# Performance work log

Measured on AMD Instinct MI355X. Metric: run time of the kernel, lower is better.

Reference implementation:

```python
import jax, jax.numpy as jnp
import numpy as np

D_MODEL, H, D_FF = 512, 8, 2048
B, S = 2, 2048
EPS = 1e-6


def _layernorm(x, alpha, beta):
    # Faithful to the torch module: unbiased std (ddof=1), eps added to STD,
    # scalar alpha/beta parameters.
    m = jnp.mean(x, axis=-1, keepdims=True)
    var = jnp.sum((x - m) ** 2, axis=-1, keepdims=True) / (x.shape[-1] - 1)
    std = jnp.sqrt(var)
    return alpha * (x - m) / (std + EPS) + beta


def _mha(x, mask, Wq, bq, Wk, bk, Wv, bv, Wo, bo):
    Bn, Sn, D = x.shape
    dk = D // H
    q = (x @ Wq + bq).reshape(Bn, Sn, H, dk).transpose(0, 2, 1, 3)  # [B,H,S,dk]
    k = (x @ Wk + bk).reshape(Bn, Sn, H, dk).transpose(0, 2, 1, 3)
    v = (x @ Wv + bv).reshape(Bn, Sn, H, dk).transpose(0, 2, 1, 3)
    scores = jnp.einsum('bhqd,bhkd->bhqk', q, k) / jnp.sqrt(jnp.float32(dk))
    scores = jnp.where(mask == 0, -jnp.inf, scores)  # mask [B,1,1,S] broadcasts
    attn = jax.nn.softmax(scores, axis=-1)
    out = jnp.einsum('bhqk,bhkd->bhqd', attn, v)
    out = out.transpose(0, 2, 1, 3).reshape(Bn, Sn, D)
    return out @ Wo + bo


def _ffn(x, W1, b1, W2, b2):
    return jax.nn.relu(x @ W1 + b1) @ W2 + b2


def setup_inputs() -> dict:
    key = jax.random.key(0)
    ks = jax.random.split(key, 12)
    sd = 1.0 / np.sqrt(D_MODEL)
    sdf = 1.0 / np.sqrt(D_FF)
    inp = {
        'x': jax.random.normal(ks[0], (B, S, D_MODEL), jnp.float32),
        'src_mask': jnp.ones((B, 1, 1, S), jnp.int32),
        'Wq': jax.random.normal(ks[1], (D_MODEL, D_MODEL), jnp.float32) * sd,
        'bq': jnp.zeros((D_MODEL,), jnp.float32),
        'Wk': jax.random.normal(ks[2], (D_MODEL, D_MODEL), jnp.float32) * sd,
        'bk': jnp.zeros((D_MODEL,), jnp.float32),
        'Wv': jax.random.normal(ks[3], (D_MODEL, D_MODEL), jnp.float32) * sd,
        'bv': jnp.zeros((D_MODEL,), jnp.float32),
        'Wo': jax.random.normal(ks[4], (D_MODEL, D_MODEL), jnp.float32) * sd,
        'bo': jnp.zeros((D_MODEL,), jnp.float32),
        'W1': jax.random.normal(ks[5], (D_MODEL, D_FF), jnp.float32) * sd,
        'b1': jnp.zeros((D_FF,), jnp.float32),
        'W2': jax.random.normal(ks[6], (D_FF, D_MODEL), jnp.float32) * sdf,
        'b2': jnp.zeros((D_MODEL,), jnp.float32),
        'alpha1': jnp.ones((1,), jnp.float32),
        'beta1': jnp.zeros((1,), jnp.float32),
        'alpha2': jnp.ones((1,), jnp.float32),
        'beta2': jnp.zeros((1,), jnp.float32),
    }
    return inp


def reference(x, src_mask, Wq, bq, Wk, bk, Wv, bv, Wo, bo,
              W1, b1, W2, b2, alpha1, beta1, alpha2, beta2):
    # SkipConnection 0: x + dropout(MHA(LN(x)))  (dropout=0 -> identity)
    h1 = _layernorm(x, alpha1, beta1)
    x = x + _mha(h1, src_mask, Wq, bq, Wk, bk, Wv, bv, Wo, bo)
    # SkipConnection 1: x + dropout(FFN(LN(x)))
    h2 = _layernorm(x, alpha2, beta2)
    x = x + _ffn(h2, W1, b1, W2, b2)
    return x
```

## Files before the change

kernel.cpp:

```cpp
#include <hip/hip_runtime.h>
#include <hip/hip_bf16.h>

typedef __hip_bfloat16 bf16;
typedef __attribute__((ext_vector_type(8))) short s8v;
typedef __attribute__((ext_vector_type(4))) float f32x4;

#define DM 512
#define NH 8
#define DKH 64
#define DFF 2048
#define NB 2
#define NS 2048
#define NR (NB*NS)
#define LN_EPS 1e-6f
#define NEG_BIG (-1e30f)
#define LDQKV (3*DM)
#define SM_SHIFT (-6.0f)
#define PART_ELEMS (NB*NH*NS*DKH)

#define MFMA_B16(a,b,c) __builtin_amdgcn_mfma_f32_16x16x32_bf16(a,b,c,0,0,0)

#define GLOAD16(g, l) __builtin_amdgcn_global_load_lds( \
    (const __attribute__((address_space(1))) void*)(g), \
    (__attribute__((address_space(3))) void*)(l), 16, 0, 0)

__device__ __forceinline__ float us2f(unsigned int u){ return __uint_as_float(u << 16); }
__device__ __forceinline__ float b2f(bf16 v){ return __bfloat162float(v); }
__device__ __forceinline__ float ldf(const float* p){ return *p; }
__device__ __forceinline__ float ldf(const bf16* p){ return __bfloat162float(*p); }
__device__ __forceinline__ void stf(float* p, float v){ *p = v; }
__device__ __forceinline__ void stf(bf16* p, float v){ *p = __float2bfloat16(v); }
__device__ __forceinline__ unsigned short f2bu(float f){
  bf16 b = __float2bfloat16(f);
  return *reinterpret_cast<unsigned short*>(&b);
}

template<int N> __device__ __forceinline__ void waitcnt_vm(){
  if constexpr(N==0)      asm volatile("s_waitcnt vmcnt(0)" ::: "memory");
  else if constexpr(N==2) asm volatile("s_waitcnt vmcnt(2)" ::: "memory");
  else if constexpr(N==3) asm volatile("s_waitcnt vmcnt(3)" ::: "memory");
  else if constexpr(N==4) asm volatile("s_waitcnt vmcnt(4)" ::: "memory");
  else if constexpr(N==6) asm volatile("s_waitcnt vmcnt(6)" ::: "memory");
  else if constexpr(N==8) asm volatile("s_waitcnt vmcnt(8)" ::: "memory");
}

__device__ __forceinline__ int swz(int row, int colbyte){
  return ((row<<7) + colbyte) ^ ((row&7)<<4);
}

__device__ __forceinline__ float wsum(float v){
#pragma unroll
  for(int o=32;o>0;o>>=1) v += __shfl_down(v,o,64);
  return v;
}

template<int NTHR>
__device__ __forceinline__ void stage_tile(char* lds, const bf16* g, int ld, int R, int tid){
  int nch = R*8;
  for(int c = tid; c < nch; c += NTHR){
    int row = c>>3;
    int blk = (c&7) ^ (row&7);
    GLOAD16(g + (size_t)row*ld + blk*8, lds + c*16);
  }
}
__device__ __forceinline__ s8v read_frag(const char* lds, int row, int col){
  return *reinterpret_cast<const s8v*>(lds + swz(row, col<<1));
}

__global__ __launch_bounds__(256) void prep_kernel(
    const float* __restrict__ Wq, const float* __restrict__ Wk,
    const float* __restrict__ Wv, const float* __restrict__ Wo,
    const float* __restrict__ W1, const float* __restrict__ W2,
    bf16* __restrict__ WTqkv, bf16* __restrict__ WTo,
    bf16* __restrict__ WT1, bf16* __restrict__ WT2,
    const float* __restrict__ x, bf16* __restrict__ h1,
    const float* __restrict__ ap, const float* __restrict__ bp){
  __shared__ float t[64][65];
  __shared__ float s1[4], s2[4];
  int tid = threadIdx.x;
  if(blockIdx.x >= 768){
    int row = blockIdx.x - 768;
    const float* xr = x + (size_t)row*DM;
    float v0 = xr[tid], v1 = xr[tid+256];
    float s = wsum(v0+v1);
    float q = wsum(v0*v0+v1*v1);
    int wid = tid>>6, lane = tid&63;
    if(lane==0){ s1[wid]=s; s2[wid]=q; }
    __syncthreads();
    float S = s1[0]+s1[1]+s1[2]+s1[3];
    float Q = s2[0]+s2[1]+s2[2]+s2[3];
    float mean = S*(1.f/DM);
    float var  = (Q - (float)DM*mean*mean)*(1.f/(DM-1));
    float sd   = sqrtf(fmaxf(var,0.f));
    float sc = (*ap)/(sd+LN_EPS);
    float b = *bp;
    bf16* orow = h1 + (size_t)row*DM;
    orow[tid]     = __float2bfloat16((v0-mean)*sc + b);
    orow[tid+256] = __float2bfloat16((v1-mean)*sc + b);
    return;
  }
  int tb = blockIdx.x;
  const float* W; bf16* WT; int K, N, nx;
  if(tb < 192){
    int w = tb>>6; tb &= 63;
    W = (w==0)?Wq:(w==1)?Wk:Wv; WT = WTqkv + w*512*512; K=512; N=512; nx=8;
  } else if(tb < 256){ tb -= 192; W=Wo; WT=WTo; K=512; N=512; nx=8; }
  else if(tb < 512){ tb -= 256; W=W1; WT=WT1; K=512; N=2048; nx=32; }
  else { tb -= 512; W=W2; WT=WT2; K=2048; N=512; nx=8; }
  int n0 = (tb % nx)*64, k0 = (tb / nx)*64;
  int rr = tid>>6, cc = tid&63;
#pragma unroll
  for(int r=rr;r<64;r+=4) t[r][cc] = W[(size_t)(k0+r)*N + n0+cc];
  __syncthreads();
#pragma unroll
  for(int r=rr;r<64;r+=4) WT[(size_t)(n0+r)*K + k0+cc] = __float2bfloat16(t[cc][r]);
}

template<typename TI>
__global__ __launch_bounds__(256) void ln_kernel(const TI* __restrict__ x,
    bf16* __restrict__ out, const float* __restrict__ ap, const float* __restrict__ bp){
  __shared__ float s1[4], s2[4];
  int row = blockIdx.x, tid = threadIdx.x;
  const TI* xr = x + (size_t)row*DM;
  float v0 = ldf(xr+tid), v1 = ldf(xr+tid+256);
  float s = wsum(v0+v1);
  float q = wsum(v0*v0+v1*v1);
  int wid = tid>>6, lane = tid&63;
  if(lane==0){ s1[wid]=s; s2[wid]=q; }
  __syncthreads();
  float S = s1[0]+s1[1]+s1[2]+s1[3];
  float Q = s2[0]+s2[1]+s2[2]+s2[3];
  float mean = S*(1.f/DM);
  float var  = (Q - (float)DM*mean*mean)*(1.f/(DM-1));
  float sd   = sqrtf(fmaxf(var,0.f));
  float sc = (*ap)/(sd+LN_EPS);
  float b = *bp;
  bf16* orow = out + (size_t)row*DM;
  orow[tid]     = __float2bfloat16((v0-mean)*sc + b);
  orow[tid+256] = __float2bfloat16((v1-mean)*sc + b);
}

template<int BM, int BN, int RELU, int QKVSEL, typename TR, typename TO>
__global__ __launch_bounds__(256) void mfma_gemm(
    const bf16* __restrict__ A, const bf16* __restrict__ WT,
    const float* __restrict__ bias0, const float* __restrict__ bias1,
    const float* __restrict__ bias2,
    const TR* __restrict__ resid, TO* __restrict__ out,
    bf16* __restrict__ vt, int M, int N, int K){
  constexpr int NW = BN/2, NF = NW/16, MI = (BM+31)/32, WRS = BM/2;
  constexpr int LOADS = BM/32 + BN/32;
  __shared__ char lA[2][BM*128];
  __shared__ char lB[2][BN*128];
  int tid = threadIdx.x, wave = tid>>6, lane = tid&63;
  int m0 = blockIdx.x*BM, n0 = blockIdx.y*BN;
  int wr = wave>>1, wc = wave&1;
  int g = lane>>4, li = lane&15;
  f32x4 acc[MI][NF] = {};
  stage_tile<256>(lA[0], A + (size_t)m0*K, K, BM, tid);
  stage_tile<256>(lB[0], WT + (size_t)n0*K, K, BN, tid);
  int NT = K>>6;
  int cur = 0;
  for(int t=0; t<NT; ++t, cur^=1){
    if(t+1 < NT){
      stage_tile<256>(lA[cur^1], A + (size_t)m0*K + (t+1)*64, K, BM, tid);
      stage_tile<256>(lB[cur^1], WT + (size_t)n0*K + (t+1)*64, K, BN, tid);
      waitcnt_vm<LOADS>();
    } else {
      waitcnt_vm<0>();
    }
    __builtin_amdgcn_sched_barrier(0);
    __builtin_amdgcn_s_barrier();
    __builtin_amdgcn_sched_barrier(0);
#pragma unroll
    for(int kk=0; kk<2; kk++){
      s8v af[MI], bfr[NF];
#pragma unroll
      for(int mi=0;mi<MI;mi++) af[mi] = read_frag(lA[cur], wr*WRS+mi*16+li, kk*32+g*8);
#pragma unroll
      for(int ni=0;ni<NF;ni++) bfr[ni] = read_frag(lB[cur], wc*NW+ni*16+li, kk*32+g*8);
#pragma unroll
      for(int mi=0;mi<MI;mi++)
#pragma unroll
        for(int ni=0;ni<NF;ni++)
          acc[mi][ni] = MFMA_B16(af[mi], bfr[ni], acc[mi][ni]);
    }
    __builtin_amdgcn_sched_barrier(0);
    __builtin_amdgcn_s_barrier();
  }
#pragma unroll
  for(int mi=0;mi<MI;mi++)
#pragma unroll
  for(int ni=0;ni<NF;ni++){
    int row = m0 + wr*WRS + mi*16 + g*4;
    int col = n0 + wc*NW + ni*16 + li;
    const float* bp = bias0;
    if(QKVSEL) bp = (col<512)? bias0 : (col<1024)? (bias1-512) : (bias2-1024);
    float bb = bp[col];
    if(QKVSEL && col >= 1024){
      int hh = (col-1024)>>6, dd = (col-1024)&63;
      int b_ = row>>11, s = row&(NS-1);
      int kb_ = s&63;
      bf16* vtp = vt + (((size_t)(b_*NH+hh)*DKH + dd)*NS + (s&~63) + (kb_>>4));
#pragma unroll
      for(int r=0;r<4;r++)
        vtp[((kb_&15)+r)*4] = __float2bfloat16(acc[mi][ni][r] + bb);
      continue;
    }
#pragma unroll
    for(int r=0;r<4;r++){
      float v = acc[mi][ni][r] + bb;
      if(RELU) v = fmaxf(v, 0.f);
      size_t off = (size_t)(row+r)*N + col;
      if(resid) v += ldf(resid+off);
      stf(out+off, v);
    }
  }
}

__global__ __launch_bounds__(512,2) void flash_attn(
    const bf16* __restrict__ QKV, const bf16* __restrict__ VT,
    const int* __restrict__ mask, bf16* __restrict__ partA,
    bf16* __restrict__ partB, float* __restrict__ lbuf){
  __shared__ char lK[2][128*128];
  __shared__ char lV[2][2][64*128];
  __shared__ char lP[8][16*128];
  int tid = threadIdx.x, wave = tid>>6, lane = tid&63;
  int bid = blockIdx.x;
  int xcd = bid & 7, u = bid >> 3;
  int q0 = (u & 15)*128;
  int bhk = xcd + 8*(u>>4);
  int h = bhk & 7, kh = (bhk>>3)&1, b = bhk>>4;
  int kbase = kh*(NS/2);
  int g = lane>>4, li = lane&15;
  const bf16* Qg  = QKV + ((size_t)b*NS + q0)*LDQKV + h*DKH;
  const bf16* Kg  = QKV + ((size_t)b*NS + kbase)*LDQKV + DM + h*DKH;
  const bf16* VTg = VT + ((size_t)(b*NH + h))*DKH*NS + kbase;
  stage_tile<512>(lK[0], Qg, LDQKV, 128, tid);
  __syncthreads();
  s8v qf0 = read_frag(lK[0], wave*16+li, g*8);
  s8v qf1 = read_frag(lK[0], wave*16+li, 32+g*8);
  __syncthreads();
  stage_tile<512>(lK[0], Kg, LDQKV, 128, tid);
  stage_tile<512>(lV[0][0], VTg,      NS, 64, tid);
  stage_tile<512>(lV[0][1], VTg + 64, NS, 64, tid);
  unsigned long long mb = 0;
#pragma unroll 16
  for(int j=0;j<64;j++)
    mb |= (unsigned long long)(mask[b*NS + kbase + j*16 + li] != 0) << j;
  __syncthreads();
  f32x4 acc[4] = {};
  f32x4 acc_l = {};
  s8v ones;
#pragma unroll
  for(int j=0;j<8;j++) ones[j] = (short)0x3F80;
  char* lPw = lP[wave];

  auto compute = [&](int t, int c){
#pragma unroll
    for(int s=0;s<2;s++){
      f32x4 S[4] = {};
      __builtin_amdgcn_s_setprio(1);
#pragma unroll
      for(int kk=0;kk<2;kk++){
        s8v qf = kk ? qf1 : qf0;
        s8v kf[4];
#pragma unroll
        for(int ni=0;ni<4;ni++) kf[ni] = read_frag(lK[c], s*64+ni*16+li, kk*32+g*8);
#pragma unroll
        for(int ni=0;ni<4;ni++)
          S[ni] = MFMA_B16(qf, kf[ni], S[ni]);
      }
      __builtin_amdgcn_s_setprio(0);
      int jb = t*8 + s*4;
      float madd[4];
#pragma unroll
      for(int ni=0;ni<4;ni++)
        madd[ni] = ((mb>>(jb+ni))&1ull) ? SM_SHIFT : NEG_BIG;
#pragma unroll
      for(int r=0;r<4;r++){
        float e0 = __expf(fmaf(S[0][r], 0.125f, madd[0]));
        float e1 = __expf(fmaf(S[1][r], 0.125f, madd[1]));
        float e2 = __expf(fmaf(S[2][r], 0.125f, madd[2]));
        float e3 = __expf(fmaf(S[3][r], 0.125f, madd[3]));
        int row = g*4 + r;
        uint2 w;
        w.x = (unsigned int)f2bu(e0) | ((unsigned int)f2bu(e1)<<16);
        w.y = (unsigned int)f2bu(e2) | ((unsigned int)f2bu(e3)<<16);
        *reinterpret_cast<uint2*>(lPw + swz(row, li<<3)) = w;
      }
      __builtin_amdgcn_s_setprio(1);
#pragma unroll
      for(int kk=0;kk<2;kk++){
        s8v pf = read_frag(lPw, li, kk*32+g*8);
        s8v vf[4];
#pragma unroll
        for(int nd=0;nd<4;nd++) vf[nd] = read_frag(lV[c][s], nd*16+li, kk*32+g*8);
#pragma unroll
        for(int nd=0;nd<4;nd++)
          acc[nd] = MFMA_B16(pf, vf[nd], acc[nd]);
        acc_l = MFMA_B16(pf, ones, acc_l);
      }
      __builtin_amdgcn_s_setprio(0);
    }
  };

  int cur = 0;
  for(int t=0; t<7; ++t, cur^=1){
    stage_tile<512>(lK[cur^1], Kg + (size_t)(t+1)*128*LDQKV, LDQKV, 128, tid);
    stage_tile<512>(lV[cur^1][0], VTg + (t+1)*128,      NS, 64, tid);
    stage_tile<512>(lV[cur^1][1], VTg + (t+1)*128 + 64, NS, 64, tid);
    waitcnt_vm<4>();
    __builtin_amdgcn_sched_barrier(0);
    __builtin_amdgcn_s_barrier();
    __builtin_amdgcn_sched_barrier(0);
    compute(t, cur);
    __builtin_amdgcn_sched_barrier(0);
    __builtin_amdgcn_s_barrier();
  }
  waitcnt_vm<0>();
  __builtin_amdgcn_sched_barrier(0);
  __builtin_amdgcn_s_barrier();
  __builtin_amdgcn_sched_barrier(0);
  compute(7, cur);

  bf16* part = kh ? partB : partA;
  size_t qb = (size_t)(b*NH + h)*NS;
#pragma unroll
  for(int r=0;r<4;r++){
    int qrow = q0 + wave*16 + g*4 + r;
#pragma unroll
    for(int nd=0;nd<4;nd++)
      part[(qb + qrow)*DKH + nd*16 + li] = __float2bfloat16(acc[nd][r]);
    if(li==0)
      lbuf[((size_t)((b*NH+h)*2 + kh))*NS + qrow] = acc_l[r];
  }
}

__global__ __launch_bounds__(256) void combine_attn(const bf16* __restrict__ pA,
    const bf16* __restrict__ pB, const float* __restrict__ lbuf,
    bf16* __restrict__ cx){
  int e = blockIdx.x*256 + threadIdx.x;
  int idx = e*4;
  int d = idx & 63, q = (idx>>6)&(NS-1), h = (idx>>17)&7, b = idx>>20;
  uint2 ua = *reinterpret_cast<const uint2*>(pA+idx);
  uint2 ub = *reinterpret_cast<const uint2*>(pB+idx);
  float lA = lbuf[((size_t)((b*NH+h)*2+0))*NS + q];
  float lB = lbuf[((size_t)((b*NH+h)*2+1))*NS + q];
  float il = 1.f/(lA+lB);
  bf16* o = cx + ((size_t)(b*NS+q)*DM + h*DKH + d);
  o[0] = __float2bfloat16((us2f(ua.x&0xffffu)+us2f(ub.x&0xffffu))*il);
  o[1] = __float2bfloat16((us2f(ua.x>>16)+us2f(ub.x>>16))*il);
  o[2] = __float2bfloat16((us2f(ua.y&0xffffu)+us2f(ub.y&0xffffu))*il);
  o[3] = __float2bfloat16((us2f(ua.y>>16)+us2f(ub.y>>16))*il);
}

extern "C" void kernel_launch(void* const* d_in, const int* in_sizes, int n_in,
                              void* d_out, int out_size, void* d_ws, size_t ws_size,
                              hipStream_t stream){
  const float* x   = (const float*)d_in[0];
  const int* mask  = (const int*)d_in[1];
  const float* Wq = (const float*)d_in[2];
  const float* bq = (const float*)d_in[3];
  const float* Wk = (const float*)d_in[4];
  const float* bk = (const float*)d_in[5];
  const float* Wv = (const float*)d_in[6];
  const float* bv = (const float*)d_in[7];
  const float* Wo = (const float*)d_in[8];
  const float* bo = (const float*)d_in[9];
  const float* W1 = (const float*)d_in[10];
  const float* b1 = (const float*)d_in[11];
  const float* W2 = (const float*)d_in[12];
  const float* b2 = (const float*)d_in[13];
  const float* a1 = (const float*)d_in[14];
  const float* be1= (const float*)d_in[15];
  const float* a2 = (const float*)d_in[16];
  const float* be2= (const float*)d_in[17];

  char* ws = (char*)d_ws;
  bf16* h1    = (bf16*)(ws);
  bf16* accA  = (bf16*)(ws);
  bf16* WTqkv = (bf16*)(ws + (size_t)( 4<<20));
  bf16* WTo   = (bf16*)(ws + (size_t)(11<<19));
  bf16* WT1   = (bf16*)(ws + (size_t)( 8<<20));
  bf16* WT2   = (bf16*)(ws + (size_t)(10<<20));
  bf16* qkv   = (bf16*)(ws + (size_t)(12<<20));
  bf16* VT    = (bf16*)(ws + (size_t)(24<<20));
  bf16* cx    = (bf16*)(ws + (size_t)(24<<20));
  bf16* x1    = h1;
  bf16* h2    = (bf16*)(ws + (size_t)( 4<<20));
  bf16* mid   = qkv;
  float* lbuf = (float*)d_out;
  bf16* accB  = (bf16*)((char*)d_out + (1<<20));

  prep_kernel<<<4864,256,0,stream>>>(Wq,Wk,Wv,Wo,W1,W2, WTqkv,WTo,WT1,WT2,
                                     x, h1, a1, be1);
  mfma_gemm<128,64,0,1,float,bf16><<<dim3(32,24),256,0,stream>>>(
      h1, WTqkv, bq, bk, bv, (const float*)nullptr, qkv, VT, NR, LDQKV, DM);
  flash_attn<<<512,512,0,stream>>>(qkv, VT, mask, accA, accB, lbuf);
  combine_attn<<<PART_ELEMS/1024,256,0,stream>>>(accA, accB, lbuf, cx);
  mfma_gemm<32,64,0,0,float,bf16><<<dim3(128,8),256,0,stream>>>(
      cx, WTo, bo, bo, bo, x, x1, (bf16*)nullptr, NR, DM, DM);
  ln_kernel<bf16><<<NR,256,0,stream>>>(x1, h2, a2, be2);
  mfma_gemm<128,128,1,0,float,bf16><<<dim3(32,16),256,0,stream>>>(
      h2, WT1, b1, b1, b1, (const float*)nullptr, mid, (bf16*)nullptr, NR, DFF, DM);
  mfma_gemm<32,64,0,0,bf16,float><<<dim3(128,8),256,0,stream>>>(
      mid, WT2, b2, b2, b2, x1, (float*)d_out, (bf16*)nullptr, NR, DM, DFF);
}
```

Baseline: 121.8 us.

## Fuse split-K attention combine into the Wo projection GEMM prologue

Removes the separate combine_attn kernel and merges the two half-key attention partials (normalized by summed l) while staging the A tile of a new dedicated Wo GEMM. This drops one launch and the write and re-read of the combined context tensor. Buffers are remapped so that WTo lives in the output buffer and the partials do not clash with other workspace. The cost is that each of the 8 column blocks recomputes the combine for the same rows, so partial reads grow eightfold, and A staging is a synchronous register load instead of an async copy.

New measurement: 119.8 us. No clear change (-1.6%).

```diff
diff --git a/kernel.cpp b/kernel.cpp
--- a/kernel.cpp
+++ b/kernel.cpp
@@ -217,6 +217,73 @@
   }
 }
 
+__global__ __launch_bounds__(256) void wo_gemm(
+    const bf16* __restrict__ pA, const bf16* __restrict__ pB,
+    const float* __restrict__ lbuf, const bf16* __restrict__ WTo,
+    const float* __restrict__ bo, const float* __restrict__ xres,
+    bf16* __restrict__ x1){
+  __shared__ char lA[2][32*128];
+  __shared__ char lB[2][64*128];
+  int tid = threadIdx.x, wave = tid>>6, lane = tid&63;
+  int m0 = blockIdx.x*32, n0 = blockIdx.y*64;
+  int wr = wave>>1, wc = wave&1;
+  int g = lane>>4, li = lane&15;
+  f32x4 acc[2] = {};
+  int r = tid>>3, blk = (tid&7)^(r&7);
+  int m = m0 + r, b_ = m>>11, q = m&(NS-1);
+
+  auto cmb = [](unsigned int ua, unsigned int ub, float il) -> unsigned int {
+    float lo = (us2f(ua&0xffffu)+us2f(ub&0xffffu))*il;
+    float hi = (us2f(ua>>16)   +us2f(ub>>16)   )*il;
+    return (unsigned int)f2bu(lo) | ((unsigned int)f2bu(hi)<<16);
+  };
+  auto stageA = [&](char* dst, int h){
+    size_t base = (((size_t)(b_*NH+h)*NS) + q)*DKH + blk*8;
+    uint4 a4 = *reinterpret_cast<const uint4*>(pA + base);
+    uint4 b4 = *reinterpret_cast<const uint4*>(pB + base);
+    float la = lbuf[((size_t)((b_*NH+h)*2+0))*NS + q];
+    float lb = lbuf[((size_t)((b_*NH+h)*2+1))*NS + q];
+    float il = 1.f/(la+lb);
+    uint4 o;
+    o.x = cmb(a4.x, b4.x, il);
+    o.y = cmb(a4.y, b4.y, il);
+    o.z = cmb(a4.z, b4.z, il);
+    o.w = cmb(a4.w, b4.w, il);
+    *reinterpret_cast<uint4*>(dst + tid*16) = o;
+  };
+
+  stageA(lA[0], 0);
+  stage_tile<256>(lB[0], WTo + (size_t)n0*DM, DM, 64, tid);
+  __syncthreads();
+  int cur = 0;
+  for(int t=0; t<8; ++t, cur^=1){
+    if(t+1 < 8){
+      stageA(lA[cur^1], t+1);
+      stage_tile<256>(lB[cur^1], WTo + (size_t)n0*DM + (t+1)*64, DM, 64, tid);
+    }
+#pragma unroll
+    for(int kk=0; kk<2; kk++){
+      s8v af = read_frag(lA[cur], wr*16+li, kk*32+g*8);
+      s8v b0 = read_frag(lB[cur], wc*32+li,    kk*32+g*8);
+      s8v b1 = read_frag(lB[cur], wc*32+16+li, kk*32+g*8);
+      acc[0] = MFMA_B16(af, b0, acc[0]);
+      acc[1] = MFMA_B16(af, b1, acc[1]);
+    }
+    __syncthreads();
+  }
+  int row = m0 + wr*16 + g*4;
+#pragma unroll
+  for(int ni=0;ni<2;ni++){
+    int col = n0 + wc*32 + ni*16 + li;
+    float bv = bo[col];
+#pragma unroll
+    for(int r2=0;r2<4;r2++){
+      size_t off = (size_t)(row+r2)*DM + col;
+      x1[off] = __float2bfloat16(acc[ni][r2] + bv + xres[off]);
+    }
+  }
+}
+
 __global__ __launch_bounds__(512,2) void flash_attn(
     const bf16* __restrict__ QKV, const bf16* __restrict__ VT,
     const int* __restrict__ mask, bf16* __restrict__ partA,
@@ -334,24 +401,6 @@
     if(li==0)
       lbuf[((size_t)((b*NH+h)*2 + kh))*NS + qrow] = acc_l[r];
   }
-}
-
-__global__ __launch_bounds__(256) void combine_attn(const bf16* __restrict__ pA,
-    const bf16* __restrict__ pB, const float* __restrict__ lbuf,
-    bf16* __restrict__ cx){
-  int e = blockIdx.x*256 + threadIdx.x;
-  int idx = e*4;
-  int d = idx & 63, q = (idx>>6)&(NS-1), h = (idx>>17)&7, b = idx>>20;
-  uint2 ua = *reinterpret_cast<const uint2*>(pA+idx);
-  uint2 ub = *reinterpret_cast<const uint2*>(pB+idx);
-  float lA = lbuf[((size_t)((b*NH+h)*2+0))*NS + q];
-  float lB = lbuf[((size_t)((b*NH+h)*2+1))*NS + q];
-  float il = 1.f/(lA+lB);
-  bf16* o = cx + ((size_t)(b*NS+q)*DM + h*DKH + d);
-  o[0] = __float2bfloat16((us2f(ua.x&0xffffu)+us2f(ub.x&0xffffu))*il);
-  o[1] = __float2bfloat16((us2f(ua.x>>16)+us2f(ub.x>>16))*il);
-  o[2] = __float2bfloat16((us2f(ua.y&0xffffu)+us2f(ub.y&0xffffu))*il);
-  o[3] = __float2bfloat16((us2f(ua.y>>16)+us2f(ub.y>>16))*il);
 }
 
 extern "C" void kernel_launch(void* const* d_in, const int* in_sizes, int n_in,
@@ -378,28 +427,25 @@
 
   char* ws = (char*)d_ws;
   bf16* h1    = (bf16*)(ws);
-  bf16* accA  = (bf16*)(ws);
+  bf16* x1    = (bf16*)(ws);
   bf16* WTqkv = (bf16*)(ws + (size_t)( 4<<20));
-  bf16* WTo   = (bf16*)(ws + (size_t)(11<<19));
+  bf16* pA    = (bf16*)(ws + (size_t)( 4<<20));
+  bf16* h2    = (bf16*)(ws + (size_t)( 4<<20));
   bf16* WT1   = (bf16*)(ws + (size_t)( 8<<20));
   bf16* WT2   = (bf16*)(ws + (size_t)(10<<20));
   bf16* qkv   = (bf16*)(ws + (size_t)(12<<20));
+  bf16* mid   = (bf16*)(ws + (size_t)(12<<20));
   bf16* VT    = (bf16*)(ws + (size_t)(24<<20));
-  bf16* cx    = (bf16*)(ws + (size_t)(24<<20));
-  bf16* x1    = h1;
-  bf16* h2    = (bf16*)(ws + (size_t)( 4<<20));
-  bf16* mid   = qkv;
   float* lbuf = (float*)d_out;
-  bf16* accB  = (bf16*)((char*)d_out + (1<<20));
+  bf16* pB    = (bf16*)((char*)d_out + (1<<20));
+  bf16* WTo   = (bf16*)((char*)d_out + (5<<20));
 
   prep_kernel<<<4864,256,0,stream>>>(Wq,Wk,Wv,Wo,W1,W2, WTqkv,WTo,WT1,WT2,
                                      x, h1, a1, be1);
   mfma_gemm<128,64,0,1,float,bf16><<<dim3(32,24),256,0,stream>>>(
       h1, WTqkv, bq, bk, bv, (const float*)nullptr, qkv, VT, NR, LDQKV, DM);
-  flash_attn<<<512,512,0,stream>>>(qkv, VT, mask, accA, accB, lbuf);
-  combine_attn<<<PART_ELEMS/1024,256,0,stream>>>(accA, accB, lbuf, cx);
-  mfma_gemm<32,64,0,0,float,bf16><<<dim3(128,8),256,0,stream>>>(
-      cx, WTo, bo, bo, bo, x, x1, (bf16*)nullptr, NR, DM, DM);
+  flash_attn<<<512,512,0,stream>>>(qkv, VT, mask, pA, pB, lbuf);
+  wo_gemm<<<dim3(128,8),256,0,stream>>>(pA, pB, lbuf, WTo, bo, x, x1);
   ln_kernel<bf16><<<NR,256,0,stream>>>(x1, h2, a2, be2);
   mfma_gemm<128,128,1,0,float,bf16><<<dim3(32,16),256,0,stream>>>(
       h2, WT1, b1, b1, b1, (const float*)nullptr, mid, (bf16*)nullptr, NR, DFF, DM);
```
